# Kernel optimization log

Hardware: AMD Instinct MI355X
Metric: run time of the kernel (lower is better)

Reference implementation:

```python
import jax, jax.numpy as jnp
import numpy as np

N = 500000
TOL = 0.01
ALPHA = 0.1
SLOPE = 0.01
EPS = 1e-10


def smooth_relu(x):
    # 0 for x<0; x^2/2 for 0<=x<1; x-1/2 for x>=1 (C1 smooth ReLU)
    return jnp.where(x < 0, 0.0, jnp.where(x < 1, 0.5 * x * x, x - 0.5))


def leaky_relu(x):
    return jnp.where(x >= 0, x, SLOPE * x)


def _xavier(key, shape):
    fan_out, fan_in = shape
    std = np.sqrt(2.0 / (fan_in + fan_out)).astype(np.float32)
    return jax.random.normal(key, shape, dtype=jnp.float32) * std


def setup_inputs() -> dict:
    key = jax.random.key(0)
    ks = jax.random.split(key, 16)
    inp = {
        'X': jax.random.normal(ks[0], (N, 2), dtype=jnp.float32),
        'Xstable': jnp.zeros((N, 2), dtype=jnp.float32),
        'Vl1_w': _xavier(ks[1], (64, 2)),
        'V2x_w': _xavier(ks[2], (64, 2)),
        'V2z_w': _xavier(ks[3], (64, 64)),
        'V3x_w': _xavier(ks[4], (64, 2)),
        'V3z_w': _xavier(ks[5], (64, 64)),
        'Vfx_w': _xavier(ks[6], (1, 2)),
        'Vfz_w': _xavier(ks[7], (1, 64)),
        'f1_w': _xavier(ks[8], (128, 2)),
        'f1_b': jnp.zeros((128,), dtype=jnp.float32),
        'f2_w': _xavier(ks[9], (128, 128)),
        'f2_b': jnp.zeros((128,), dtype=jnp.float32),
        'f3_w': _xavier(ks[10], (128, 128)),
        'f3_b': jnp.zeros((128,), dtype=jnp.float32),
        'f4_w': _xavier(ks[11], (128, 128)),
        'f4_b': jnp.zeros((128,), dtype=jnp.float32),
        'f5_w': _xavier(ks[12], (128, 128)),
        'f5_b': jnp.zeros((128,), dtype=jnp.float32),
        'ff_w': _xavier(ks[13], (2, 128)),
        'ff_b': jnp.zeros((2,), dtype=jnp.float32),
    }
    return inp


def _V_forward(X, Xstable, Vl1_w, V2x_w, V2z_w, V3x_w, V3z_w, Vfx_w, Vfz_w):
    d = X - Xstable                                  # [N,2]
    z1 = smooth_relu(d @ Vl1_w.T)                    # [N,64]
    z2 = smooth_relu(d @ V2x_w.T + z1 @ V2z_w.T)     # [N,64]
    z3 = smooth_relu(d @ V3x_w.T + z2 @ V3z_w.T)     # [N,64]
    zf = smooth_relu(d @ Vfx_w.T + z3 @ Vfz_w.T)     # [N,1]
    vsum = TOL * jnp.sum(d * d, axis=1, keepdims=True)
    return smooth_relu(zf) + vsum                    # [N,1]


def _fhat_forward(X, f1_w, f1_b, f2_w, f2_b, f3_w, f3_b, f4_w, f4_b, f5_w, f5_b, ff_w, ff_b):
    h = leaky_relu(X @ f1_w.T + f1_b)
    h = leaky_relu(h @ f2_w.T + f2_b)
    h = leaky_relu(h @ f3_w.T + f3_b)
    h = leaky_relu(h @ f4_w.T + f4_b)
    h = leaky_relu(h @ f5_w.T + f5_b)
    return h @ ff_w.T + ff_b                         # [N,2]


def reference(X, Xstable, Vl1_w, V2x_w, V2z_w, V3x_w, V3z_w, Vfx_w, Vfz_w,
              f1_w, f1_b, f2_w, f2_b, f3_w, f3_b, f4_w, f4_b, f5_w, f5_b, ff_w, ff_b):
    def Vfn(Xv):
        return _V_forward(Xv, Xstable, Vl1_w, V2x_w, V2z_w, V3x_w, V3z_w, Vfx_w, Vfz_w)

    V, pullback = jax.vjp(Vfn, X)
    gradV = pullback(jnp.ones_like(V))[0]            # dV/dX, [N,2]

    f_hat = _fhat_forward(X, f1_w, f1_b, f2_w, f2_b, f3_w, f3_b,
                          f4_w, f4_b, f5_w, f5_b, ff_w, ff_b)

    Vnorm = jnp.sum(gradV * gradV, axis=1, keepdims=True)      # [N,1]
    fh_V = jnp.sum(f_hat * gradV, axis=1, keepdims=True)       # [N,1]
    f_mul = jax.nn.relu(fh_V + ALPHA * V) / (Vnorm + EPS)      # [N,1]
    f = f_hat - gradV * f_mul                                  # [N,2]
    return f
```

## Files before the change

### kernel.cpp

```cpp
#include <hip/hip_runtime.h>


typedef _Float16 v2h __attribute__((ext_vector_type(2)));
typedef __fp16   v2hf __attribute__((ext_vector_type(2)));
typedef _Float16 v4h __attribute__((ext_vector_type(4)));
typedef _Float16 v8h __attribute__((ext_vector_type(8)));
typedef float    v4f __attribute__((ext_vector_type(4)));

__device__ __forceinline__ v2h cvt_pk(float a, float b){
  v2hf r = __builtin_amdgcn_cvt_pkrtz(a, b);
  union { v2hf f; v2h h; } u; u.f = r;
  return u.h;
}

#define NPTS 500000
#define FH_BLK  ((NPTS + 127) / 128)
#define FUSED_GRID (FH_BLK * 2)

#define BAR_LDS() asm volatile("s_waitcnt lgkmcnt(0)\n\ts_barrier" ::: "memory")

#define OFF_FW    0
#define OFF_V2Z   65536
#define OFF_V3Z   69632
#define OFF_V2ZT  73728
#define OFF_V3ZT  77824
#define OFF_VL1T  81920
#define OFF_V2XT  82048
#define OFF_V3XT  82176
#define OFF_VFZ   82304
#define OFF_FFW   82368
#define OFF_F1W   82624
#define OFF_F1P   82880
#define W16_DATA  86976
#define W16_TOTAL (W16_DATA + 2048)

__device__ __align__(16) _Float16 g_w16[W16_TOTAL];
__device__ __align__(16) float    g_fh[NPTS * 2];
__device__ __align__(16) float4   g_grad[NPTS];

#if defined(__has_builtin)
#if __has_builtin(__builtin_amdgcn_fdot2)
#define FDOT2(a,b,c) __builtin_amdgcn_fdot2((a),(b),(c),false)
#endif
#endif
#ifndef FDOT2
__device__ __forceinline__ float fdot2_fb(v2h a, v2h b, float c){
  return fmaf((float)a.x, (float)b.x, fmaf((float)a.y, (float)b.y, c));
}
#define FDOT2(a,b,c) fdot2_fb((a),(b),(c))
#endif

__device__ __forceinline__ float srelu(float x){
  float c = fminf(fmaxf(x, 0.f), 1.f);
  return c * fmaf(-0.5f, c, x);
}
__device__ __forceinline__ float sreluD(float x){
  return fminf(fmaxf(x, 0.f), 1.f);
}
__device__ __forceinline__ float sreluD_from_z(float z){
  return fminf(sqrtf(2.f * z), 1.f);
}

__device__ __forceinline__ v2h lrelu_pk(float a, float b){
  v2h x = cvt_pk(a, b);
  v2h m = x * (v2h){(_Float16)0.01f, (_Float16)0.01f};
  return __builtin_elementwise_max(x, m);
}
__device__ __forceinline__ v2h srelu_pk(float a, float b){
  v2h x = cvt_pk(a, b);
  const v2h z0 = (v2h){(_Float16)0.f, (_Float16)0.f};
  const v2h o1 = (v2h){(_Float16)1.f, (_Float16)1.f};
  const v2h hf = (v2h){(_Float16)0.5f, (_Float16)0.5f};
  v2h c = __builtin_elementwise_min(__builtin_elementwise_max(x, z0), o1);
  v2h t = x - c * hf;
  return c * t;
}

__global__ __launch_bounds__(256) void prep_kernel(
  const float* __restrict__ f2w, const float* __restrict__ f3w,
  const float* __restrict__ f4w, const float* __restrict__ f5w,
  const float* __restrict__ V2z, const float* __restrict__ V3z,
  const float* __restrict__ Vl1, const float* __restrict__ V2x,
  const float* __restrict__ V3x, const float* __restrict__ Vfz,
  const float* __restrict__ ffw, const float* __restrict__ f1w)
{
  const int i = blockIdx.x * 256 + threadIdx.x;
  if (i >= W16_TOTAL) return;
  if (i >= W16_DATA){ g_w16[i] = (_Float16)0.f; return; }
  float v;
  if (i < 65536){
    const float* W[4] = {f2w, f3w, f4w, f5w};
    v = W[i >> 14][i & 16383];
  } else if (i < 69632)  v = V2z[i - 65536];
  else if (i < 73728)    v = V3z[i - 69632];
  else if (i < 77824){ int r = i - 73728; v = V2z[(r & 63)*64 + (r >> 6)]; }
  else if (i < 81920){ int r = i - 77824; v = V3z[(r & 63)*64 + (r >> 6)]; }
  else if (i < 82048){ int r = i - 81920; v = Vl1[(r & 63)*2 + (r >> 6)]; }
  else if (i < 82176){ int r = i - 82048; v = V2x[(r & 63)*2 + (r >> 6)]; }
  else if (i < 82304){ int r = i - 82176; v = V3x[(r & 63)*2 + (r >> 6)]; }
  else if (i < 82368)    v = Vfz[i - 82304];
  else if (i < 82624)    v = ffw[i - 82368];
  else if (i < 82880)    v = f1w[i - 82624];
  else { int r = i - 82880; int k = r & 31; v = (k < 2) ? f1w[(r >> 5)*2 + k] : 0.f; }
  g_w16[i] = (_Float16)v;
}

__device__ __forceinline__ void fh_layer(_Float16* H,
    const _Float16* __restrict__ Wl, const float* __restrict__ Bp,
    int w, int lm, int q)
{
  const v4f bva = *(const v4f*)(Bp + w*32 + q*4);
  const v4f bvb = *(const v4f*)(Bp + w*32 + 16 + q*4);
  v4f acc[2][8];
#pragma unroll
  for (int nt = 0; nt < 8; ++nt){
    acc[0][nt] = bva;
    acc[1][nt] = bvb;
  }

#pragma unroll
  for (int kt = 0; kt < 4; ++kt){
    const int sw = ((kt*4 + q) ^ lm) << 3;
    v8h A0 = *(const v8h*)(Wl + (w*32      + lm)*128 + kt*32 + q*8);
    v8h A1 = *(const v8h*)(Wl + (w*32 + 16 + lm)*128 + kt*32 + q*8);
#pragma unroll
    for (int nt = 0; nt < 8; ++nt){
      v8h B = *(const v8h*)(H + (nt*16 + lm)*128 + sw);
      acc[0][nt] = __builtin_amdgcn_mfma_f32_16x16x32_f16(A0, B, acc[0][nt], 0,0,0);
      acc[1][nt] = __builtin_amdgcn_mfma_f32_16x16x32_f16(A1, B, acc[1][nt], 0,0,0);
    }
  }
  BAR_LDS();
#pragma unroll
  for (int mt = 0; mt < 2; ++mt){
    const int o0 = w*32 + mt*16 + q*4;
    const int coff = (((o0 >> 3) ^ lm) << 3) + (o0 & 7);
#pragma unroll
    for (int nt = 0; nt < 8; ++nt){
      v4h hv;
      *(v2h*)&hv       = lrelu_pk(acc[mt][nt][0], acc[mt][nt][1]);
      *((v2h*)&hv + 1) = lrelu_pk(acc[mt][nt][2], acc[mt][nt][3]);
      *(v4h*)(H + (nt*16 + lm)*128 + coff) = hv;
    }
  }
  BAR_LDS();
}

__device__ __forceinline__ void fhat_body(int b, _Float16* H,
  const float* __restrict__ X,
  const float* __restrict__ f1b, const float* __restrict__ f2b,
  const float* __restrict__ f3b, const float* __restrict__ f4b,
  const float* __restrict__ f5b, const float* __restrict__ ffb)
{
  const int t  = threadIdx.x;
  const int w  = t >> 6;
  const int l  = t & 63;
  const int lm = l & 15;
  const int q  = l >> 4;
  const int row0 = b*128 + w*32;

  {
    int r0 = row0 + lm;      if (r0 > NPTS-1) r0 = NPTS-1;
    int r1 = row0 + 16 + lm; if (r1 > NPTS-1) r1 = NPTS-1;
    const float2 x0 = *(const float2*)(X + r0*2);
    const float2 x1 = *(const float2*)(X + r1*2);
    v8h Bx0 = (v8h){(_Float16)0.f,(_Float16)0.f,(_Float16)0.f,(_Float16)0.f,
                    (_Float16)0.f,(_Float16)0.f,(_Float16)0.f,(_Float16)0.f};
    v8h Bx1 = Bx0;
    if (q == 0){
      Bx0[0] = (_Float16)x0.x; Bx0[1] = (_Float16)x0.y;
      Bx1[0] = (_Float16)x1.x; Bx1[1] = (_Float16)x1.y;
    }
#pragma unroll
    for (int mt = 0; mt < 8; ++mt){
      const int o0 = mt*16 + q*4;
      const v4f bv = *(const v4f*)(f1b + o0);
      v8h A = *(const v8h*)(g_w16 + OFF_F1P + (mt*16 + lm)*32 + q*8);
      v4f a0 = __builtin_amdgcn_mfma_f32_16x16x32_f16(A, Bx0, bv, 0,0,0);
      v4f a1 = __builtin_amdgcn_mfma_f32_16x16x32_f16(A, Bx1, bv, 0,0,0);
      const int coff = (((o0 >> 3) ^ lm) << 3) + (o0 & 7);
      v4h h0, h1;
      *(v2h*)&h0       = lrelu_pk(a0[0], a0[1]);
      *((v2h*)&h0 + 1) = lrelu_pk(a0[2], a0[3]);
      *(v2h*)&h1       = lrelu_pk(a1[0], a1[1]);
      *((v2h*)&h1 + 1) = lrelu_pk(a1[2], a1[3]);
      *(v4h*)(H + (w*32 + lm)*128 + coff)      = h0;
      *(v4h*)(H + (w*32 + 16 + lm)*128 + coff) = h1;
    }
  }
  BAR_LDS();

  fh_layer(H, g_w16 + OFF_FW,         f2b, w, lm, q);
  fh_layer(H, g_w16 + OFF_FW + 16384, f3b, w, lm, q);
  fh_layer(H, g_w16 + OFF_FW + 32768, f4b, w, lm, q);
  fh_layer(H, g_w16 + OFF_FW + 49152, f5b, w, lm, q);

  {
    v4f a0 = (v4f){0.f,0.f,0.f,0.f};
    v4f a1 = (v4f){0.f,0.f,0.f,0.f};
#pragma unroll
    for (int kt = 0; kt < 4; ++kt){
      const int sw = ((kt*4 + q) ^ lm) << 3;
      v8h A  = *(const v8h*)(g_w16 + OFF_FFW + lm*128 + kt*32 + q*8);
      v8h B0 = *(const v8h*)(H + (w*32 + lm)*128 + sw);
      v8h B1 = *(const v8h*)(H + (w*32 + 16 + lm)*128 + sw);
      a0 = __builtin_amdgcn_mfma_f32_16x16x32_f16(A, B0, a0, 0,0,0);
      a1 = __builtin_amdgcn_mfma_f32_16x16x32_f16(A, B1, a1, 0,0,0);
    }
    if (q == 0){
      const float fb0 = ffb[0], fb1 = ffb[1];
      const int r0 = row0 + lm, r1 = row0 + 16 + lm;
      if (r0 < NPTS) *(float2*)(g_fh + r0*2) = make_float2(a0[0] + fb0, a0[1] + fb1);
      if (r1 < NPTS) *(float2*)(g_fh + r1*2) = make_float2(a1[0] + fb0, a1[1] + fb1);
    }
  }
}

__device__ __forceinline__ void vfwd2_l2(_Float16* zoutA, _Float16* zoutB,
    const _Float16* __restrict__ Wz,
    const _Float16* __restrict__ WxT,
    const _Float16* __restrict__ Wl1T,
    float dA0, float dA1, float dB0, float dB1, int lm, int q)
{
  v4f accA[4], accB[4];
#pragma unroll
  for (int mt = 0; mt < 4; ++mt){
    accA[mt] = (v4f){0.f,0.f,0.f,0.f};
    accB[mt] = (v4f){0.f,0.f,0.f,0.f};
  }
  const int rs = lm & 7;
#pragma unroll
  for (int kt = 0; kt < 2; ++kt){
    v8h w0 = *(const v8h*)(Wl1T + kt*32 + q*8);
    v8h w1 = *(const v8h*)(Wl1T + 64 + kt*32 + q*8);
    v8h BA, BB;
#pragma unroll
    for (int j2 = 0; j2 < 4; ++j2){
      const float a0 = (float)w0[2*j2  ], a1 = (float)w0[2*j2+1];
      const float c0 = (float)w1[2*j2  ], c1 = (float)w1[2*j2+1];
      ((v2h*)&BA)[j2] = srelu_pk(fmaf(dA0,a0,dA1*c0), fmaf(dA0,a1,dA1*c1));
      ((v2h*)&BB)[j2] = srelu_pk(fmaf(dB0,a0,dB1*c0), fmaf(dB0,a1,dB1*c1));
    }
#pragma unroll
    for (int mt = 0; mt < 4; ++mt){
      v8h A = *(const v8h*)(Wz + (mt*16 + lm)*64 + kt*32 + q*8);
      accA[mt] = __builtin_amdgcn_mfma_f32_16x16x32_f16(A, BA, accA[mt], 0,0,0);
      accB[mt] = __builtin_amdgcn_mfma_f32_16x16x32_f16(A, BB, accB[mt], 0,0,0);
    }
  }
#pragma unroll
  for (int mt = 0; mt < 4; ++mt){
    const int o0 = mt*16 + q*4;
    const int off = (((o0 >> 3) ^ rs) << 3) + (o0 & 7);
    float vA[4], vB[4];
#pragma unroll
    for (int reg = 0; reg < 4; ++reg){
      const float wx0 = (float)WxT[o0 + reg];
      const float wx1 = (float)WxT[64 + o0 + reg];
      vA[reg] = accA[mt][reg] + wx0*dA0 + wx1*dA1;
      vB[reg] = accB[mt][reg] + wx0*dB0 + wx1*dB1;
    }
    v4h hA, hB;
    *(v2h*)&hA       = srelu_pk(vA[0], vA[1]);
    *((v2h*)&hA + 1) = srelu_pk(vA[2], vA[3]);
    *(v2h*)&hB       = srelu_pk(vB[0], vB[1]);
    *((v2h*)&hB + 1) = srelu_pk(vB[2], vB[3]);
    *(v4h*)(zoutA + lm*64 + off) = hA;
    *(v4h*)(zoutB + lm*64 + off) = hB;
  }
}

__device__ __forceinline__ void vfwd2(const _Float16* zinA, _Float16* zoutA,
    const _Float16* zinB, _Float16* zoutB,
    const _Float16* __restrict__ Wz, const _Float16* __restrict__ WxT,
    float dA0, float dA1, float dB0, float dB1, int lm, int q)
{
  v4f accA[4], accB[4];
#pragma unroll
  for (int mt = 0; mt < 4; ++mt){
    accA[mt] = (v4f){0.f,0.f,0.f,0.f};
    accB[mt] = (v4f){0.f,0.f,0.f,0.f};
  }
  const int rs = lm & 7;
#pragma unroll
  for (int kt = 0; kt < 2; ++kt){
    const int sw = (((kt*4 + q) ^ rs) << 3);
    v8h BA = *(const v8h*)(zinA + lm*64 + sw);
    v8h BB = *(const v8h*)(zinB + lm*64 + sw);
#pragma unroll
    for (int mt = 0; mt < 4; ++mt){
      v8h A = *(const v8h*)(Wz + (mt*16 + lm)*64 + kt*32 + q*8);
      accA[mt] = __builtin_amdgcn_mfma_f32_16x16x32_f16(A, BA, accA[mt], 0,0,0);
      accB[mt] = __builtin_amdgcn_mfma_f32_16x16x32_f16(A, BB, accB[mt], 0,0,0);
    }
  }
#pragma unroll
  for (int mt = 0; mt < 4; ++mt){
    const int o0 = mt*16 + q*4;
    const int off = (((o0 >> 3) ^ rs) << 3) + (o0 & 7);
    float vA[4], vB[4];
#pragma unroll
    for (int reg = 0; reg < 4; ++reg){
      const float wx0 = (float)WxT[o0 + reg];
      const float wx1 = (float)WxT[64 + o0 + reg];
      vA[reg] = accA[mt][reg] + wx0*dA0 + wx1*dA1;
      vB[reg] = accB[mt][reg] + wx0*dB0 + wx1*dB1;
    }
    v4h hA, hB;
    *(v2h*)&hA       = srelu_pk(vA[0], vA[1]);
    *((v2h*)&hA + 1) = srelu_pk(vA[2], vA[3]);
    *(v2h*)&hB       = srelu_pk(vB[0], vB[1]);
    *((v2h*)&hB + 1) = srelu_pk(vB[2], vB[3]);
    *(v4h*)(zoutA + lm*64 + off) = hA;
    *(v4h*)(zoutB + lm*64 + off) = hB;
  }
}

__device__ __forceinline__ void vbwd2(const _Float16* ginA, _Float16* zioA,
    const _Float16* ginB, _Float16* zioB,
    const _Float16* __restrict__ WT, int lm, int q)
{
  v4f accA[4], accB[4];
#pragma unroll
  for (int mt = 0; mt < 4; ++mt){
    accA[mt] = (v4f){0.f,0.f,0.f,0.f};
    accB[mt] = (v4f){0.f,0.f,0.f,0.f};
  }
  const int rs = lm & 7;
#pragma unroll
  for (int kt = 0; kt < 2; ++kt){
    const int sw = (((kt*4 + q) ^ rs) << 3);
    v8h BA = *(const v8h*)(ginA + lm*64 + sw);
    v8h BB = *(const v8h*)(ginB + lm*64 + sw);
#pragma unroll
    for (int mt = 0; mt < 4; ++mt){
      v8h A = *(const v8h*)(WT + (mt*16 + lm)*64 + kt*32 + q*8);
      accA[mt] = __builtin_amdgcn_mfma_f32_16x16x32_f16(A, BA, accA[mt], 0,0,0);
      accB[mt] = __builtin_amdgcn_mfma_f32_16x16x32_f16(A, BB, accB[mt], 0,0,0);
    }
  }
#pragma unroll
  for (int mt = 0; mt < 4; ++mt){
    const int k0 = mt*16 + q*4;
    const int off = (((k0 >> 3) ^ rs) << 3) + (k0 & 7);
    _Float16* pA = zioA + lm*64 + off;
    _Float16* pB = zioB + lm*64 + off;
    v4h zA = *(const v4h*)pA;
    v4h zB = *(const v4h*)pB;
    float sA0 = accA[mt][0] * sreluD_from_z((float)zA[0]);
    float sA1 = accA[mt][1] * sreluD_from_z((float)zA[1]);
    float sA2 = accA[mt][2] * sreluD_from_z((float)zA[2]);
    float sA3 = accA[mt][3] * sreluD_from_z((float)zA[3]);
    float sB0 = accB[mt][0] * sreluD_from_z((float)zB[0]);
    float sB1 = accB[mt][1] * sreluD_from_z((float)zB[1]);
    float sB2 = accB[mt][2] * sreluD_from_z((float)zB[2]);
    float sB3 = accB[mt][3] * sreluD_from_z((float)zB[3]);
    v4h gA, gB;
    *(v2h*)&gA       = cvt_pk(sA0, sA1);
    *((v2h*)&gA + 1) = cvt_pk(sA2, sA3);
    *(v2h*)&gB       = cvt_pk(sB0, sB1);
    *((v2h*)&gB + 1) = cvt_pk(sB2, sB3);
    *(v4h*)pA = gA;
    *(v4h*)pB = gB;
  }
}

__device__ __forceinline__ void vbwd2_l1(_Float16* zioA, _Float16* zioB,
    const _Float16* __restrict__ WT,
    const _Float16* __restrict__ Wl1T,
    float dA0, float dA1, float dB0, float dB1, int lm, int q)
{
  v4f accA[4], accB[4];
#pragma unroll
  for (int mt = 0; mt < 4; ++mt){
    accA[mt] = (v4f){0.f,0.f,0.f,0.f};
    accB[mt] = (v4f){0.f,0.f,0.f,0.f};
  }
  const int rs = lm & 7;
#pragma unroll
  for (int kt = 0; kt < 2; ++kt){
    const int sw = (((kt*4 + q) ^ rs) << 3);
    v8h BA = *(const v8h*)(zioA + lm*64 + sw);
    v8h BB = *(const v8h*)(zioB + lm*64 + sw);
#pragma unroll
    for (int mt = 0; mt < 4; ++mt){
      v8h A = *(const v8h*)(WT + (mt*16 + lm)*64 + kt*32 + q*8);
      accA[mt] = __builtin_amdgcn_mfma_f32_16x16x32_f16(A, BA, accA[mt], 0,0,0);
      accB[mt] = __builtin_amdgcn_mfma_f32_16x16x32_f16(A, BB, accB[mt], 0,0,0);
    }
  }
#pragma unroll
  for (int mt = 0; mt < 4; ++mt){
    const int k0 = mt*16 + q*4;
    const int off = (((k0 >> 3) ^ rs) << 3) + (k0 & 7);
    v4h w0 = *(const v4h*)(Wl1T + k0);
    v4h w1 = *(const v4h*)(Wl1T + 64 + k0);
    float sA[4], sB[4];
#pragma unroll
    for (int reg = 0; reg < 4; ++reg){
      const float a1A = fmaf(dA0, (float)w0[reg], dA1 * (float)w1[reg]);
      const float a1B = fmaf(dB0, (float)w0[reg], dB1 * (float)w1[reg]);
      sA[reg] = accA[mt][reg] * sreluD(a1A);
      sB[reg] = accB[mt][reg] * sreluD(a1B);
    }
    v4h gA, gB;
    *(v2h*)&gA       = cvt_pk(sA[0], sA[1]);
    *((v2h*)&gA + 1) = cvt_pk(sA[2], sA[3]);
    *(v2h*)&gB       = cvt_pk(sB[0], sB[1]);
    *((v2h*)&gB + 1) = cvt_pk(sB[2], sB[3]);
    *(v4h*)(zioA + lm*64 + off) = gA;
    *(v4h*)(zioB + lm*64 + off) = gB;
  }
}

__device__ __forceinline__ void gacc2(v4f& aGA, v4f& aGB,
    const _Float16* __restrict__ WxTbase,
    const _Float16* ZA, const _Float16* ZB, int lm, int q)
{
  const int rs = lm & 7;
#pragma unroll
  for (int kt = 0; kt < 2; ++kt){
    const int sw = (((kt*4 + q) ^ rs) << 3);
    v8h A  = *(const v8h*)(WxTbase + lm*64 + kt*32 + q*8);
    v8h BA = *(const v8h*)(ZA + lm*64 + sw);
    v8h BB = *(const v8h*)(ZB + lm*64 + sw);
    aGA = __builtin_amdgcn_mfma_f32_16x16x32_f16(A, BA, aGA, 0,0,0);
    aGB = __builtin_amdgcn_mfma_f32_16x16x32_f16(A, BB, aGB, 0,0,0);
  }
}

__device__ __forceinline__ void vnet_body2(int b, char* smem,
  const float* __restrict__ X, const float* __restrict__ Xst,
  const float* __restrict__ Vfx)
{
  const int t  = threadIdx.x;
  const int w  = t >> 6;
  const int l  = t & 63;
  const int lm = l & 15;
  const int q  = l >> 4;
  const int rs = lm & 7;

  _Float16* const ZA2 = (_Float16*)(smem + w*8192);
  _Float16* const ZA3 = ZA2 + 1024;
  _Float16* const ZB2 = ZA2 + 2048;
  _Float16* const ZB3 = ZA2 + 3072;

  const int rowA = b*128 + w*32 + lm;
  const int rowB = rowA + 16;
  const int rcA = rowA < NPTS ? rowA : NPTS-1;
  const int rcB = rowB < NPTS ? rowB : NPTS-1;
  const float2 xA = *(const float2*)(X   + rcA*2);
  const float2 sA = *(const float2*)(Xst + rcA*2);
  const float2 xB = *(const float2*)(X   + rcB*2);
  const float2 sB = *(const float2*)(Xst + rcB*2);
  const float dA0 = xA.x - sA.x, dA1 = xA.y - sA.y;
  const float dB0 = xB.x - sB.x, dB1 = xB.y - sB.y;
  const float vfx0 = Vfx[0], vfx1 = Vfx[1];

  vfwd2_l2(ZA2, ZB2, g_w16 + OFF_V2Z, g_w16 + OFF_V2XT, g_w16 + OFF_VL1T,
           dA0, dA1, dB0, dB1, lm, q);
  vfwd2(ZA2, ZA3, ZB2, ZB3, g_w16 + OFF_V3Z, g_w16 + OFF_V3XT,
        dA0, dA1, dB0, dB1, lm, q);

  float VVrA, sfA, VVrB, sfB;
  {
    v4f aSA = (v4f){0.f,0.f,0.f,0.f};
    v4f aSB = (v4f){0.f,0.f,0.f,0.f};
#pragma unroll
    for (int kt = 0; kt < 2; ++kt){
      const int sw = (((kt*4 + q) ^ rs) << 3);
      v8h A  = *(const v8h*)(g_w16 + OFF_VFZ + lm*64 + kt*32 + q*8);
      v8h BA = *(const v8h*)(ZA3 + lm*64 + sw);
      v8h BB = *(const v8h*)(ZB3 + lm*64 + sw);
      aSA = __builtin_amdgcn_mfma_f32_16x16x32_f16(A, BA, aSA, 0,0,0);
      aSB = __builtin_amdgcn_mfma_f32_16x16x32_f16(A, BB, aSB, 0,0,0);
    }
    const float afA = fmaf(vfx0, dA0, fmaf(vfx1, dA1, aSA[0]));
    const float zfA = srelu(afA);
    VVrA = srelu(zfA) + 0.01f * fmaf(dA0, dA0, dA1*dA1);
    sfA  = sreluD(zfA) * sreluD(afA);
    const float afB = fmaf(vfx0, dB0, fmaf(vfx1, dB1, aSB[0]));
    const float zfB = srelu(afB);
    VVrB = srelu(zfB) + 0.01f * fmaf(dB0, dB0, dB1*dB1);
    sfB  = sreluD(zfB) * sreluD(afB);
  }

#pragma unroll
  for (int cc = 0; cc < 2; ++cc){
    const int c = q*2 + cc;
    const int sw = ((c ^ rs) << 3);
    v8h vf = *(const v8h*)(g_w16 + OFF_VFZ + c*8);
    _Float16* pA = ZA3 + lm*64 + sw;
    _Float16* pB = ZB3 + lm*64 + sw;
    v8h zA = *(const v8h*)pA;
    v8h zB = *(const v8h*)pB;
    v8h uA, uB;
#pragma unroll
    for (int j2 = 0; j2 < 4; ++j2){
      float a0 = (float)vf[2*j2  ] * sreluD_from_z((float)zA[2*j2  ]);
      float a1 = (float)vf[2*j2+1] * sreluD_from_z((float)zA[2*j2+1]);
      float b0 = (float)vf[2*j2  ] * sreluD_from_z((float)zB[2*j2  ]);
      float b1 = (float)vf[2*j2+1] * sreluD_from_z((float)zB[2*j2+1]);
      ((v2h*)&uA)[j2] = cvt_pk(a0, a1);
      ((v2h*)&uB)[j2] = cvt_pk(b0, b1);
    }
    *(v8h*)pA = uA;
    *(v8h*)pB = uB;
  }

  v4f aGA = (v4f){0.f,0.f,0.f,0.f};
  v4f aGB = (v4f){0.f,0.f,0.f,0.f};

  gacc2(aGA, aGB, g_w16 + OFF_V3XT, ZA3, ZB3, lm, q);
  vbwd2(ZA3, ZA2, ZB3, ZB2, g_w16 + OFF_V3ZT, lm, q);
  gacc2(aGA, aGB, g_w16 + OFF_V2XT, ZA2, ZB2, lm, q);
  vbwd2_l1(ZA2, ZB2, g_w16 + OFF_V2ZT, g_w16 + OFF_VL1T,
           dA0, dA1, dB0, dB1, lm, q);
  gacc2(aGA, aGB, g_w16 + OFF_VL1T, ZA2, ZB2, lm, q);

  const float g0A = fmaf(0.02f, dA0, sfA * (vfx0 + aGA[0]));
  const float g1A = fmaf(0.02f, dA1, sfA * (vfx1 + aGA[1]));
  const float g0B = fmaf(0.02f, dB0, sfB * (vfx0 + aGB[0]));
  const float g1B = fmaf(0.02f, dB1, sfB * (vfx1 + aGB[1]));

  if (q == 0){
    if (rowA < NPTS) g_grad[rowA] = make_float4(g0A, g1A, VVrA, 0.f);
    if (rowB < NPTS) g_grad[rowB] = make_float4(g0B, g1B, VVrB, 0.f);
  }
}

__global__ __launch_bounds__(256, 4) void fused_kernel(
  const float* __restrict__ X, const float* __restrict__ Xst,
  const float* __restrict__ Vfx,
  const float* __restrict__ f1b, const float* __restrict__ f2b,
  const float* __restrict__ f3b, const float* __restrict__ f4b,
  const float* __restrict__ f5b, const float* __restrict__ ffb)
{
  __shared__ __align__(16) char smem[32768];
  const int g = blockIdx.x;
  if ((g & 1) == 0){
    fhat_body(g >> 1, (_Float16*)smem, X, f1b, f2b, f3b, f4b, f5b, ffb);
  } else {
    vnet_body2(g >> 1, smem, X, Xst, Vfx);
  }
}

__global__ __launch_bounds__(256) void combine_kernel(float* __restrict__ out)
{
  const int idx = blockIdx.x * 256 + threadIdx.x;
  const int i0 = idx * 2;
  if (i0 >= NPTS) return;
  const float4 fh2 = *(const float4*)(g_fh + i0*2);
  const float4 ga = g_grad[i0];
  const float4 gb = g_grad[i0 + 1];
  float4 o;
  {
    const float Vn  = fmaf(ga.x, ga.x, ga.y*ga.y);
    const float num = fmaf(0.1f, ga.z, fmaf(fh2.x, ga.x, fh2.y*ga.y));
    const float fm  = fmaxf(num, 0.f) / (Vn + 1e-10f);
    o.x = fmaf(-ga.x, fm, fh2.x);
    o.y = fmaf(-ga.y, fm, fh2.y);
  }
  {
    const float Vn  = fmaf(gb.x, gb.x, gb.y*gb.y);
    const float num = fmaf(0.1f, gb.z, fmaf(fh2.z, gb.x, fh2.w*gb.y));
    const float fm  = fmaxf(num, 0.f) / (Vn + 1e-10f);
    o.z = fmaf(-gb.x, fm, fh2.z);
    o.w = fmaf(-gb.y, fm, fh2.w);
  }
  *(float4*)(out + i0*2) = o;
}

extern "C" void kernel_launch(void* const* d_in, const int* in_sizes, int n_in,
                              void* d_out, int out_size, void* d_ws, size_t ws_size,
                              hipStream_t stream)
{
  (void)d_ws; (void)ws_size; (void)n_in; (void)in_sizes; (void)out_size;
  const float* X   = (const float*)d_in[0];
  const float* Xst = (const float*)d_in[1];
  const float* Vl1 = (const float*)d_in[2];
  const float* V2x = (const float*)d_in[3];
  const float* V2z = (const float*)d_in[4];
  const float* V3x = (const float*)d_in[5];
  const float* V3z = (const float*)d_in[6];
  const float* Vfx = (const float*)d_in[7];
  const float* Vfz = (const float*)d_in[8];
  const float* f1w = (const float*)d_in[9];
  const float* f1b = (const float*)d_in[10];
  const float* f2w = (const float*)d_in[11];
  const float* f2b = (const float*)d_in[12];
  const float* f3w = (const float*)d_in[13];
  const float* f3b = (const float*)d_in[14];
  const float* f4w = (const float*)d_in[15];
  const float* f4b = (const float*)d_in[16];
  const float* f5w = (const float*)d_in[17];
  const float* f5b = (const float*)d_in[18];
  const float* ffw = (const float*)d_in[19];
  const float* ffb = (const float*)d_in[20];

  prep_kernel<<<(W16_TOTAL + 255)/256, 256, 0, stream>>>(
      f2w, f3w, f4w, f5w, V2z, V3z, Vl1, V2x, V3x, Vfz, ffw, f1w);
  fused_kernel<<<FUSED_GRID, 256, 0, stream>>>(
      X, Xst, Vfx, f1b, f2b, f3b, f4b, f5b, ffb);
  combine_kernel<<<(NPTS/2 + 255)/256, 256, 0, stream>>>((float*)d_out);
}
```

Baseline: 272.6 us.

## Fuse f_hat, V-net and combine into a single per-block kernel

Each block now computes the f_hat MLP and then the V-network forward/backward for the same 128 rows, keeping f_hat in registers and producing the final output directly. This drops the global g_fh/g_grad intermediates and the separate combine kernel launch. The trade-off is serialization of the two sub-networks within one block instead of interleaved independent blocks, which halves the grid and may reduce latency hiding; register pressure also rises because f_hat values stay live through the V-net.

```diff
diff --git a/kernel.cpp b/kernel.cpp
--- a/kernel.cpp
+++ b/kernel.cpp
@@ -14,8 +14,7 @@
 }
 
 #define NPTS 500000
-#define FH_BLK  ((NPTS + 127) / 128)
-#define FUSED_GRID (FH_BLK * 2)
+#define FUSED_GRID ((NPTS + 127) / 128)
 
 #define BAR_LDS() asm volatile("s_waitcnt lgkmcnt(0)\n\ts_barrier" ::: "memory")
 
@@ -35,20 +34,6 @@
 #define W16_TOTAL (W16_DATA + 2048)
 
 __device__ __align__(16) _Float16 g_w16[W16_TOTAL];
-__device__ __align__(16) float    g_fh[NPTS * 2];
-__device__ __align__(16) float4   g_grad[NPTS];
-
-#if defined(__has_builtin)
-#if __has_builtin(__builtin_amdgcn_fdot2)
-#define FDOT2(a,b,c) __builtin_amdgcn_fdot2((a),(b),(c),false)
-#endif
-#endif
-#ifndef FDOT2
-__device__ __forceinline__ float fdot2_fb(v2h a, v2h b, float c){
-  return fmaf((float)a.x, (float)b.x, fmaf((float)a.y, (float)b.y, c));
-}
-#define FDOT2(a,b,c) fdot2_fb((a),(b),(c))
-#endif
 
 __device__ __forceinline__ float srelu(float x){
   float c = fminf(fmaxf(x, 0.f), 1.f);
@@ -144,76 +129,6 @@
     }
   }
   BAR_LDS();
-}
-
-__device__ __forceinline__ void fhat_body(int b, _Float16* H,
-  const float* __restrict__ X,
-  const float* __restrict__ f1b, const float* __restrict__ f2b,
-  const float* __restrict__ f3b, const float* __restrict__ f4b,
-  const float* __restrict__ f5b, const float* __restrict__ ffb)
-{
-  const int t  = threadIdx.x;
-  const int w  = t >> 6;
-  const int l  = t & 63;
-  const int lm = l & 15;
-  const int q  = l >> 4;
-  const int row0 = b*128 + w*32;
-
-  {
-    int r0 = row0 + lm;      if (r0 > NPTS-1) r0 = NPTS-1;
-    int r1 = row0 + 16 + lm; if (r1 > NPTS-1) r1 = NPTS-1;
-    const float2 x0 = *(const float2*)(X + r0*2);
-    const float2 x1 = *(const float2*)(X + r1*2);
-    v8h Bx0 = (v8h){(_Float16)0.f,(_Float16)0.f,(_Float16)0.f,(_Float16)0.f,
-                    (_Float16)0.f,(_Float16)0.f,(_Float16)0.f,(_Float16)0.f};
-    v8h Bx1 = Bx0;
-    if (q == 0){
-      Bx0[0] = (_Float16)x0.x; Bx0[1] = (_Float16)x0.y;
-      Bx1[0] = (_Float16)x1.x; Bx1[1] = (_Float16)x1.y;
-    }
-#pragma unroll
-    for (int mt = 0; mt < 8; ++mt){
-      const int o0 = mt*16 + q*4;
-      const v4f bv = *(const v4f*)(f1b + o0);
-      v8h A = *(const v8h*)(g_w16 + OFF_F1P + (mt*16 + lm)*32 + q*8);
-      v4f a0 = __builtin_amdgcn_mfma_f32_16x16x32_f16(A, Bx0, bv, 0,0,0);
-      v4f a1 = __builtin_amdgcn_mfma_f32_16x16x32_f16(A, Bx1, bv, 0,0,0);
-      const int coff = (((o0 >> 3) ^ lm) << 3) + (o0 & 7);
-      v4h h0, h1;
-      *(v2h*)&h0       = lrelu_pk(a0[0], a0[1]);
-      *((v2h*)&h0 + 1) = lrelu_pk(a0[2], a0[3]);
-      *(v2h*)&h1       = lrelu_pk(a1[0], a1[1]);
-      *((v2h*)&h1 + 1) = lrelu_pk(a1[2], a1[3]);
-      *(v4h*)(H + (w*32 + lm)*128 + coff)      = h0;
-      *(v4h*)(H + (w*32 + 16 + lm)*128 + coff) = h1;
-    }
-  }
-  BAR_LDS();
-
-  fh_layer(H, g_w16 + OFF_FW,         f2b, w, lm, q);
-  fh_layer(H, g_w16 + OFF_FW + 16384, f3b, w, lm, q);
-  fh_layer(H, g_w16 + OFF_FW + 32768, f4b, w, lm, q);
-  fh_layer(H, g_w16 + OFF_FW + 49152, f5b, w, lm, q);
-
-  {
-    v4f a0 = (v4f){0.f,0.f,0.f,0.f};
-    v4f a1 = (v4f){0.f,0.f,0.f,0.f};
-#pragma unroll
-    for (int kt = 0; kt < 4; ++kt){
-      const int sw = ((kt*4 + q) ^ lm) << 3;
-      v8h A  = *(const v8h*)(g_w16 + OFF_FFW + lm*128 + kt*32 + q*8);
-      v8h B0 = *(const v8h*)(H + (w*32 + lm)*128 + sw);
-      v8h B1 = *(const v8h*)(H + (w*32 + 16 + lm)*128 + sw);
-      a0 = __builtin_amdgcn_mfma_f32_16x16x32_f16(A, B0, a0, 0,0,0);
-      a1 = __builtin_amdgcn_mfma_f32_16x16x32_f16(A, B1, a1, 0,0,0);
-    }
-    if (q == 0){
-      const float fb0 = ffb[0], fb1 = ffb[1];
-      const int r0 = row0 + lm, r1 = row0 + 16 + lm;
-      if (r0 < NPTS) *(float2*)(g_fh + r0*2) = make_float2(a0[0] + fb0, a0[1] + fb1);
-      if (r1 < NPTS) *(float2*)(g_fh + r1*2) = make_float2(a1[0] + fb0, a1[1] + fb1);
-    }
-  }
 }
 
 __device__ __forceinline__ void vfwd2_l2(_Float16* zoutA, _Float16* zoutB,
@@ -429,32 +344,92 @@
   }
 }
 
-__device__ __forceinline__ void vnet_body2(int b, char* smem,
+__global__ __launch_bounds__(256, 4) void fused_kernel(
   const float* __restrict__ X, const float* __restrict__ Xst,
-  const float* __restrict__ Vfx)
-{
+  const float* __restrict__ Vfx,
+  const float* __restrict__ f1b, const float* __restrict__ f2b,
+  const float* __restrict__ f3b, const float* __restrict__ f4b,
+  const float* __restrict__ f5b, const float* __restrict__ ffb,
+  float* __restrict__ out)
+{
+  __shared__ __align__(16) char smem[32768];
+  _Float16* const H = (_Float16*)smem;
+
+  const int b  = blockIdx.x;
   const int t  = threadIdx.x;
   const int w  = t >> 6;
   const int l  = t & 63;
   const int lm = l & 15;
   const int q  = l >> 4;
   const int rs = lm & 7;
+  const int row0 = b*128 + w*32;
+
+  const int r0 = row0 + lm;
+  const int r1 = row0 + 16 + lm;
+  const int rc0 = r0 < NPTS ? r0 : NPTS-1;
+  const int rc1 = r1 < NPTS ? r1 : NPTS-1;
+  const float2 x0 = *(const float2*)(X + rc0*2);
+  const float2 x1 = *(const float2*)(X + rc1*2);
+
+  {
+    v8h Bx0 = (v8h){(_Float16)0.f,(_Float16)0.f,(_Float16)0.f,(_Float16)0.f,
+                    (_Float16)0.f,(_Float16)0.f,(_Float16)0.f,(_Float16)0.f};
+    v8h Bx1 = Bx0;
+    if (q == 0){
+      Bx0[0] = (_Float16)x0.x; Bx0[1] = (_Float16)x0.y;
+      Bx1[0] = (_Float16)x1.x; Bx1[1] = (_Float16)x1.y;
+    }
+#pragma unroll
+    for (int mt = 0; mt < 8; ++mt){
+      const int o0 = mt*16 + q*4;
+      const v4f bv = *(const v4f*)(f1b + o0);
+      v8h A = *(const v8h*)(g_w16 + OFF_F1P + (mt*16 + lm)*32 + q*8);
+      v4f a0 = __builtin_amdgcn_mfma_f32_16x16x32_f16(A, Bx0, bv, 0,0,0);
+      v4f a1 = __builtin_amdgcn_mfma_f32_16x16x32_f16(A, Bx1, bv, 0,0,0);
+      const int coff = (((o0 >> 3) ^ lm) << 3) + (o0 & 7);
+      v4h h0, h1;
+      *(v2h*)&h0       = lrelu_pk(a0[0], a0[1]);
+      *((v2h*)&h0 + 1) = lrelu_pk(a0[2], a0[3]);
+      *(v2h*)&h1       = lrelu_pk(a1[0], a1[1]);
+      *((v2h*)&h1 + 1) = lrelu_pk(a1[2], a1[3]);
+      *(v4h*)(H + (w*32 + lm)*128 + coff)      = h0;
+      *(v4h*)(H + (w*32 + 16 + lm)*128 + coff) = h1;
+    }
+  }
+  BAR_LDS();
+
+  fh_layer(H, g_w16 + OFF_FW,         f2b, w, lm, q);
+  fh_layer(H, g_w16 + OFF_FW + 16384, f3b, w, lm, q);
+  fh_layer(H, g_w16 + OFF_FW + 32768, f4b, w, lm, q);
+  fh_layer(H, g_w16 + OFF_FW + 49152, f5b, w, lm, q);
+
+  float fhA0, fhA1, fhB0, fhB1;
+  {
+    v4f a0 = (v4f){0.f,0.f,0.f,0.f};
+    v4f a1 = (v4f){0.f,0.f,0.f,0.f};
+#pragma unroll
+    for (int kt = 0; kt < 4; ++kt){
+      const int sw = ((kt*4 + q) ^ lm) << 3;
+      v8h A  = *(const v8h*)(g_w16 + OFF_FFW + lm*128 + kt*32 + q*8);
+      v8h B0 = *(const v8h*)(H + (w*32 + lm)*128 + sw);
+      v8h B1 = *(const v8h*)(H + (w*32 + 16 + lm)*128 + sw);
+      a0 = __builtin_amdgcn_mfma_f32_16x16x32_f16(A, B0, a0, 0,0,0);
+      a1 = __builtin_amdgcn_mfma_f32_16x16x32_f16(A, B1, a1, 0,0,0);
+    }
+    const float fb0 = ffb[0], fb1 = ffb[1];
+    fhA0 = a0[0] + fb0; fhA1 = a0[1] + fb1;
+    fhB0 = a1[0] + fb0; fhB1 = a1[1] + fb1;
+  }
 
   _Float16* const ZA2 = (_Float16*)(smem + w*8192);
   _Float16* const ZA3 = ZA2 + 1024;
   _Float16* const ZB2 = ZA2 + 2048;
   _Float16* const ZB3 = ZA2 + 3072;
 
-  const int rowA = b*128 + w*32 + lm;
-  const int rowB = rowA + 16;
-  const int rcA = rowA < NPTS ? rowA : NPTS-1;
-  const int rcB = rowB < NPTS ? rowB : NPTS-1;
-  const float2 xA = *(const float2*)(X   + rcA*2);
-  const float2 sA = *(const float2*)(Xst + rcA*2);
-  const float2 xB = *(const float2*)(X   + rcB*2);
-  const float2 sB = *(const float2*)(Xst + rcB*2);
-  const float dA0 = xA.x - sA.x, dA1 = xA.y - sA.y;
-  const float dB0 = xB.x - sB.x, dB1 = xB.y - sB.y;
+  const float2 sA = *(const float2*)(Xst + rc0*2);
+  const float2 sB = *(const float2*)(Xst + rc1*2);
+  const float dA0 = x0.x - sA.x, dA1 = x0.y - sA.y;
+  const float dB0 = x1.x - sB.x, dB1 = x1.y - sB.y;
   const float vfx0 = Vfx[0], vfx1 = Vfx[1];
 
   vfwd2_l2(ZA2, ZB2, g_w16 + OFF_V2Z, g_w16 + OFF_V2XT, g_w16 + OFF_VL1T,
@@ -524,51 +499,21 @@
   const float g1B = fmaf(0.02f, dB1, sfB * (vfx1 + aGB[1]));
 
   if (q == 0){
-    if (rowA < NPTS) g_grad[rowA] = make_float4(g0A, g1A, VVrA, 0.f);
-    if (rowB < NPTS) g_grad[rowB] = make_float4(g0B, g1B, VVrB, 0.f);
-  }
-}
-
-__global__ __launch_bounds__(256, 4) void fused_kernel(
-  const float* __restrict__ X, const float* __restrict__ Xst,
-  const float* __restrict__ Vfx,
-  const float* __restrict__ f1b, const float* __restrict__ f2b,
-  const float* __restrict__ f3b, const float* __restrict__ f4b,
-  const float* __restrict__ f5b, const float* __restrict__ ffb)
-{
-  __shared__ __align__(16) char smem[32768];
-  const int g = blockIdx.x;
-  if ((g & 1) == 0){
-    fhat_body(g >> 1, (_Float16*)smem, X, f1b, f2b, f3b, f4b, f5b, ffb);
-  } else {
-    vnet_body2(g >> 1, smem, X, Xst, Vfx);
-  }
-}
-
-__global__ __launch_bounds__(256) void combine_kernel(float* __restrict__ out)
-{
-  const int idx = blockIdx.x * 256 + threadIdx.x;
-  const int i0 = idx * 2;
-  if (i0 >= NPTS) return;
-  const float4 fh2 = *(const float4*)(g_fh + i0*2);
-  const float4 ga = g_grad[i0];
-  const float4 gb = g_grad[i0 + 1];
-  float4 o;
-  {
-    const float Vn  = fmaf(ga.x, ga.x, ga.y*ga.y);
-    const float num = fmaf(0.1f, ga.z, fmaf(fh2.x, ga.x, fh2.y*ga.y));
-    const float fm  = fmaxf(num, 0.f) / (Vn + 1e-10f);
-    o.x = fmaf(-ga.x, fm, fh2.x);
-    o.y = fmaf(-ga.y, fm, fh2.y);
-  }
-  {
-    const float Vn  = fmaf(gb.x, gb.x, gb.y*gb.y);
-    const float num = fmaf(0.1f, gb.z, fmaf(fh2.z, gb.x, fh2.w*gb.y));
-    const float fm  = fmaxf(num, 0.f) / (Vn + 1e-10f);
-    o.z = fmaf(-gb.x, fm, fh2.z);
-    o.w = fmaf(-gb.y, fm, fh2.w);
-  }
-  *(float4*)(out + i0*2) = o;
+    if (r0 < NPTS){
+      const float Vn  = fmaf(g0A, g0A, g1A*g1A);
+      const float num = fmaf(0.1f, VVrA, fmaf(fhA0, g0A, fhA1*g1A));
+      const float fm  = fmaxf(num, 0.f) / (Vn + 1e-10f);
+      *(float2*)(out + r0*2) =
+        make_float2(fmaf(-g0A, fm, fhA0), fmaf(-g1A, fm, fhA1));
+    }
+    if (r1 < NPTS){
+      const float Vn  = fmaf(g0B, g0B, g1B*g1B);
+      const float num = fmaf(0.1f, VVrB, fmaf(fhB0, g0B, fhB1*g1B));
+      const float fm  = fmaxf(num, 0.f) / (Vn + 1e-10f);
+      *(float2*)(out + r1*2) =
+        make_float2(fmaf(-g0B, fm, fhB0), fmaf(-g1B, fm, fhB1));
+    }
+  }
 }
 
 extern "C" void kernel_launch(void* const* d_in, const int* in_sizes, int n_in,
@@ -601,6 +546,5 @@
   prep_kernel<<<(W16_TOTAL + 255)/256, 256, 0, stream>>>(
       f2w, f3w, f4w, f5w, V2z, V3z, Vl1, V2x, V3x, Vfz, ffw, f1w);
   fused_kernel<<<FUSED_GRID, 256, 0, stream>>>(
-      X, Xst, Vfx, f1b, f2b, f3b, f4b, f5b, ffb);
-  combine_kernel<<<(NPTS/2 + 255)/256, 256, 0, stream>>>((float*)d_out);
-}
+      X, Xst, Vfx, f1b, f2b, f3b, f4b, f5b, ffb, (float*)d_out);
+}
```

After: 271.0 us. About the same (-0.6%).
